# Optimization experiments

Measured on AMD Instinct MI355X. Metric: run time of the kernel, lower is better.

Reference implementation:

```python
import jax, jax.numpy as jnp
import numpy as np

BOS = 1          # BOS_TOK_IDX
PAD = 0          # PAD_TOK_IDX (embedding padding row zeroed)
NL = 2           # n_layers (both decoder and encoder)
H_DEC = 1024     # decoder hidden = enc.emb_size
H_ENC = 512      # encoder hidden per direction (out_size = 1024)


def lstm_cell(x, h, c, Wih, Whh, bih, bhh):
    # PyTorch gate order: i, f, g, o
    gates = x @ Wih.T + h @ Whh.T + bih + bhh
    i, f, g, o = jnp.split(gates, 4, axis=-1)
    c = jax.nn.sigmoid(f) * c + jax.nn.sigmoid(i) * jnp.tanh(g)
    h = jax.nn.sigmoid(o) * jnp.tanh(c)
    return h, c


def setup_inputs() -> dict:
    key = jax.random.key(0)
    ks = jax.random.split(key, 20)
    B, T_ENC, V, E = 32, 128, 32000, 512
    sd = 1.0 / np.sqrt(H_DEC)
    se = 1.0 / np.sqrt(H_ENC)
    u = lambda k, shape, s: jax.random.uniform(k, shape, jnp.float32, -s, s)
    emb_W = jax.random.normal(ks[0], (V, E), jnp.float32)
    emb_W = emb_W.at[PAD].set(0.0)  # padding_idx
    return {
        "enc_outs": jax.random.normal(ks[1], (B, T_ENC, 2 * H_ENC), jnp.float32),
        "enc_h": 0.1 * jax.random.normal(ks[2], (NL, B, H_DEC), jnp.float32),
        "enc_c": 0.1 * jax.random.normal(ks[3], (NL, B, H_DEC), jnp.float32),
        "max_len": 256,
        "emb_W": emb_W,
        # decoder LSTM (unidirectional, 2 layers; layer0 in=E, layer1 in=H_DEC)
        "dec_Wih0": u(ks[4], (4 * H_DEC, E), sd),
        "dec_Whh0": u(ks[5], (4 * H_DEC, H_DEC), sd),
        "dec_bih0": u(ks[6], (4 * H_DEC,), sd),
        "dec_bhh0": u(ks[7], (4 * H_DEC,), sd),
        "dec_Wih1": u(ks[8], (4 * H_DEC, H_DEC), sd),
        "dec_Whh1": u(ks[9], (4 * H_DEC, H_DEC), sd),
        "dec_bih1": u(ks[10], (4 * H_DEC,), sd),
        "dec_bhh1": u(ks[11], (4 * H_DEC,), sd),
        # encoder biLSTM, stacked [layer, dir]; input dim 1024 for both layers
        "enc_Wih": u(ks[12], (NL, 2, 4 * H_ENC, 2 * H_ENC), se),
        "enc_Whh": u(ks[13], (NL, 2, 4 * H_ENC, H_ENC), se),
        "enc_bih": u(ks[14], (NL, 2, 4 * H_ENC), se),
        "enc_bhh": u(ks[15], (NL, 2, 4 * H_ENC), se),
    }


def _run_dir(x, Wih, Whh, bih, bhh, reverse):
    # x: [B, T, D] -> ys: [B, T, H], final (h, c)
    B = x.shape[0]
    H = Whh.shape[-1]
    z = jnp.zeros((B, H), dtype=x.dtype)

    def step(carry, xt):
        h, c = lstm_cell(xt, carry[0], carry[1], Wih, Whh, bih, bhh)
        return (h, c), h

    (hT, cT), ys = jax.lax.scan(step, (z, z), jnp.swapaxes(x, 0, 1), reverse=reverse)
    return jnp.swapaxes(ys, 0, 1), hT, cT


def reference(enc_outs, enc_h, enc_c, max_len, emb_W,
              dec_Wih0, dec_Whh0, dec_bih0, dec_bhh0,
              dec_Wih1, dec_Whh1, dec_bih1, dec_bhh1,
              enc_Wih, enc_Whh, enc_bih, enc_bhh):
    B = enc_outs.shape[0]
    # dec_inps is never updated in the loop: always the BOS embedding (eval dropout = id)
    x0 = jnp.broadcast_to(emb_W[BOS], (B, emb_W.shape[1]))

    def dec_step(carry, _):
        h0, c0, h1, c1 = carry
        h0, c0 = lstm_cell(x0, h0, c0, dec_Wih0, dec_Whh0, dec_bih0, dec_bhh0)
        h1, c1 = lstm_cell(h0, h1, c1, dec_Wih1, dec_Whh1, dec_bih1, dec_bhh1)
        return (h0, c0, h1, c1), h1

    init = (enc_h[0], enc_c[0], enc_h[1], enc_c[1])
    _, result = jax.lax.scan(dec_step, init, None, length=max_len)  # [T, B, H_DEC]
    out = jnp.swapaxes(result, 0, 1)  # [B, T, H_DEC]

    # bidirectional encoder over the decoded sequence (pre_embedded, full lengths)
    for l in range(NL):
        yf, hf, cf = _run_dir(out, enc_Wih[l, 0], enc_Whh[l, 0], enc_bih[l, 0], enc_bhh[l, 0], False)
        yb, hb, cb = _run_dir(out, enc_Wih[l, 1], enc_Whh[l, 1], enc_bih[l, 1], enc_bhh[l, 1], True)
        out = jnp.concatenate([yf, yb], axis=-1)

    # to_dec_state: concat last-layer fwd/bwd states, expand over n_layers
    lnhn = jnp.concatenate([hf, hb], axis=1)  # [B, out_size]
    lncn = jnp.concatenate([cf, cb], axis=1)
    dec_h = jnp.broadcast_to(lnhn, (NL,) + lnhn.shape)
    dec_c = jnp.broadcast_to(lncn, (NL,) + lncn.shape)
    return out, dec_h, dec_c
```

## Files before the change

kernel.cpp:

```cpp
#include <hip/hip_runtime.h>


typedef _Float16 f16;
typedef _Float16 hvec8 __attribute__((ext_vector_type(8)));
typedef float fvec4 __attribute__((ext_vector_type(4)));

#define WS_H0   4096
#define WS_H1   135168
#define WS_HE   266240
#define WS_DEC  397312
#define WS_Y0   17174528

__device__ __forceinline__ fvec4 mf(hvec8 a, hvec8 b, fvec4 c) {
    return __builtin_amdgcn_mfma_f32_16x16x32_f16(a, b, c, 0, 0, 0);
}

__device__ __forceinline__ hvec8 ldb8(const float* p) {
    hvec8 h;
#pragma unroll
    for (int j = 0; j < 8; ++j) h[j] = (f16)p[j];
    return h;
}

__device__ __forceinline__ hvec8 lda8(const f16* p) {
    hvec8 v;
    asm volatile("global_load_dwordx4 %0, %1, off sc1" : "=v"(v) : "v"(p));
    return v;
}
__device__ __forceinline__ void vm_wait() {
    asm volatile("s_waitcnt vmcnt(0)" ::: "memory");
    __builtin_amdgcn_sched_barrier(0);
}

__device__ __forceinline__ void st2(f16* p, float a, float b) {
    union { f16 h[2]; unsigned u; } x;
    x.h[0] = (f16)a; x.h[1] = (f16)b;
    __hip_atomic_store((unsigned*)p, x.u, __ATOMIC_RELAXED, __HIP_MEMORY_SCOPE_AGENT);
}

__device__ __forceinline__ float sigf(float x) { return 1.f / (1.f + __expf(-x)); }
__device__ __forceinline__ float thf(float x) {
    x = fminf(15.f, fmaxf(-15.f, x));
    float e = __expf(2.f * x);
    return (e - 1.f) / (e + 1.f);
}

#define RED(t, m, w, n)  red[(((t)*16 + (m))*132) + ((w)*16) + (n)]
#define RED2(t, m, n)    red2[(((t)*16 + (m))*20) + (n)]

__global__ void __launch_bounds__(512, 1)
seq2seq_kernel(const float* __restrict__ enc_h, const float* __restrict__ enc_c,
               const float* __restrict__ emb_W,
               const float* __restrict__ dWih0, const float* __restrict__ dWhh0,
               const float* __restrict__ dbih0, const float* __restrict__ dbhh0,
               const float* __restrict__ dWih1, const float* __restrict__ dWhh1,
               const float* __restrict__ dbih1, const float* __restrict__ dbhh1,
               const float* __restrict__ eWih, const float* __restrict__ eWhh,
               const float* __restrict__ ebih, const float* __restrict__ ebhh,
               float* __restrict__ out, char* __restrict__ ws)
{
    const int tid  = threadIdx.x;
    const int wave = tid >> 6, lane = tid & 63;
    const int wg   = blockIdx.x;
    const int bg   = wg >> 7;
    const int g    = wg & 127;
    const int n16  = lane & 15;
    const int kq   = (lane >> 4) * 8;

    unsigned* flags  = (unsigned*)ws;
    unsigned* myflag = flags + (size_t)wg * 4;

    f16* H0  = (f16*)(ws + WS_H0);
    f16* H1  = (f16*)(ws + WS_H1);
    f16* HE  = (f16*)(ws + WS_HE);
    f16* DEC = (f16*)(ws + WS_DEC);
    f16* Y0  = (f16*)(ws + WS_Y0);

    __shared__ float red[64 * 132];
    __shared__ float red2[64 * 20];
    __shared__ float cdec[2][8][16];
    __shared__ float cenc[8][16];
    __shared__ float pre0_l[32];
    __shared__ float bias1_l[32];
    __shared__ float biasE_l[32];

    unsigned cnt = 0;
    auto bar = [&](int base, int two) {
        const unsigned tgt = ++cnt;
        __syncthreads();
        if (wave == 0) {
            if (lane == 0)
                __hip_atomic_store(myflag, tgt, __ATOMIC_RELAXED, __HIP_MEMORY_SCOPE_AGENT);
            const unsigned* p0 = flags + (size_t)(base + lane) * 4;
            const unsigned* p1 = p0 + 64 * 4;
            for (;;) {
                unsigned a = __hip_atomic_load(p0, __ATOMIC_RELAXED, __HIP_MEMORY_SCOPE_AGENT);
                if (two) {
                    unsigned b = __hip_atomic_load(p1, __ATOMIC_RELAXED, __HIP_MEMORY_SCOPE_AGENT);
                    a = (a < b) ? a : b;
                }
                if (__all((int)(a >= tgt))) break;
                __builtin_amdgcn_s_sleep(2);
            }
        }
        __syncthreads();
    };

    const int u0 = g * 8;
    hvec8 bL0[2][4], bL1[2][8];
    {
        const int gate = n16 >> 2, uu = n16 & 3;
#pragma unroll
        for (int t = 0; t < 2; ++t) {
            const int r = gate * 1024 + u0 + t * 4 + uu;
#pragma unroll
            for (int s = 0; s < 4; ++s)
                bL0[t][s] = ldb8(dWhh0 + (size_t)r * 1024 + wave * 128 + s * 32 + kq);
#pragma unroll
            for (int s = 0; s < 8; ++s) {
                const int k1 = wave * 256 + s * 32;
                bL1[t][s] = (k1 < 1024)
                    ? ldb8(dWih1 + (size_t)r * 1024 + k1 + kq)
                    : ldb8(dWhh1 + (size_t)r * 1024 + (k1 - 1024) + kq);
            }
        }
    }
    if (tid < 128) {
        const int which = tid >> 6, q = tid & 63, j = q >> 4, m = q & 15;
        const int b = bg * 16 + m, u = u0 + 2 * j;
        const float* src_c = enc_c + (size_t)(which * 32 + b) * 1024 + u;
        const float* src_h = enc_h + (size_t)(which * 32 + b) * 1024 + u;
        cdec[which][2 * j][m]     = src_c[0];
        cdec[which][2 * j + 1][m] = src_c[1];
        f16* dst = which ? H1 : H0;
        st2(dst + (size_t)(32 + b) * 1024 + u, src_h[0], src_h[1]);
    }
    if (tid < 32) {
        const int t = tid >> 4, nn = tid & 15;
        const int r = (nn >> 2) * 1024 + u0 + t * 4 + (nn & 3);
        const float* x0 = emb_W + 512;
        float s = dbih0[r] + dbhh0[r];
        const float* wr = dWih0 + (size_t)r * 512;
        for (int k = 0; k < 512; ++k) s += wr[k] * x0[k];
        pre0_l[tid]  = s;
        bias1_l[tid] = dbih1[r] + dbhh1[r];
    }
    bar(bg * 128, 1);

    for (int tau = 0; tau <= 256; ++tau) {
        const int prd = (tau + 1) & 1;
        const int pwr = tau & 1;
        fvec4 acc[4];
#pragma unroll
        for (int i = 0; i < 4; ++i) acc[i] = 0;
        const int m = n16;
        hvec8 a0f[4], a1f[8];
        if (tau < 256) {
            const f16* a0 = H0 + (size_t)(prd * 32 + bg * 16 + m) * 1024 + wave * 128 + kq;
#pragma unroll
            for (int s = 0; s < 4; ++s) a0f[s] = lda8(a0 + s * 32);
        }
        if (tau >= 1) {
            const f16* a1 = (wave < 4)
                ? H0 + (size_t)(prd * 32 + bg * 16 + m) * 1024 + wave * 256 + kq
                : H1 + (size_t)(pwr * 32 + bg * 16 + m) * 1024 + (wave - 4) * 256 + kq;
#pragma unroll
            for (int s = 0; s < 8; ++s) a1f[s] = lda8(a1 + s * 32);
        }
        vm_wait();
        if (tau < 256) {
#pragma unroll
            for (int s = 0; s < 4; ++s) {
                acc[0] = mf(a0f[s], bL0[0][s], acc[0]);
                acc[1] = mf(a0f[s], bL0[1][s], acc[1]);
            }
        }
        if (tau >= 1) {
#pragma unroll
            for (int s = 0; s < 8; ++s) {
                acc[2] = mf(a1f[s], bL1[0][s], acc[2]);
                acc[3] = mf(a1f[s], bL1[1][s], acc[3]);
            }
        }
        {
            const int mg = lane >> 4;
#pragma unroll
            for (int t = 0; t < 4; ++t)
#pragma unroll
                for (int r = 0; r < 4; ++r)
                    RED(t, mg * 4 + r, wave, n16) = acc[t][r];
        }
        __syncthreads();
        for (int it = tid; it < 1024; it += 512) {
            const int t = it >> 8, mm = it & 15, nn = (it >> 4) & 15;
            const float* p = &RED(t, mm, 0, nn);
            RED2(t, mm, nn) = ((p[0] + p[16]) + (p[32] + p[48]))
                            + ((p[64] + p[80]) + (p[96] + p[112]));
        }
        __syncthreads();
        if (tid < 64 && tau < 256) {
            const int j = tid >> 4, m2 = tid & 15, t = j >> 1;
            float hh[2];
#pragma unroll
            for (int e = 0; e < 2; ++e) {
                const int uu = 2 * j + e, ul = uu & 3;
                const float gi = RED2(t, m2, ul)      + pre0_l[t * 16 + ul];
                const float gf = RED2(t, m2, 4 + ul)  + pre0_l[t * 16 + 4 + ul];
                const float gg = RED2(t, m2, 8 + ul)  + pre0_l[t * 16 + 8 + ul];
                const float go = RED2(t, m2, 12 + ul) + pre0_l[t * 16 + 12 + ul];
                float c = cdec[0][uu][m2];
                c = sigf(gf) * c + sigf(gi) * thf(gg);
                hh[e] = sigf(go) * thf(c);
                cdec[0][uu][m2] = c;
            }
            st2(H0 + (size_t)(pwr * 32 + bg * 16 + m2) * 1024 + u0 + 2 * j, hh[0], hh[1]);
        }
        if (tid >= 64 && tid < 128 && tau >= 1) {
            const int q = tid - 64;
            const int j = q >> 4, m2 = q & 15, t = j >> 1;
            float hh[2];
#pragma unroll
            for (int e = 0; e < 2; ++e) {
                const int uu = 2 * j + e, ul = uu & 3;
                const float gi = RED2(2 + t, m2, ul)      + bias1_l[t * 16 + ul];
                const float gf = RED2(2 + t, m2, 4 + ul)  + bias1_l[t * 16 + 4 + ul];
                const float gg = RED2(2 + t, m2, 8 + ul)  + bias1_l[t * 16 + 8 + ul];
                const float go = RED2(2 + t, m2, 12 + ul) + bias1_l[t * 16 + 12 + ul];
                float c = cdec[1][uu][m2];
                c = sigf(gf) * c + sigf(gi) * thf(gg);
                hh[e] = sigf(go) * thf(c);
                cdec[1][uu][m2] = c;
            }
            const int b = bg * 16 + m2, u = u0 + 2 * j;
            st2(H1 + (size_t)(prd * 32 + b) * 1024 + u, hh[0], hh[1]);
            st2(DEC + ((size_t)(tau - 1) * 32 + b) * 1024 + u, hh[0], hh[1]);
        }
        bar(bg * 128, 1);
    }

    const int dir = g >> 6;
    const int ge  = g & 63;
    const int ue0 = ge * 8;
    const int dbase = bg * 128 + dir * 64;
    for (int l = 0; l < 2; ++l) {
        hvec8 bE[2][6];
        {
            const int gate = n16 >> 2, uu = n16 & 3;
            const float* Wih = eWih + (size_t)(l * 2 + dir) * 2048 * 1024;
            const float* Whh = eWhh + (size_t)(l * 2 + dir) * 2048 * 512;
#pragma unroll
            for (int t = 0; t < 2; ++t) {
                const int r = gate * 512 + ue0 + t * 4 + uu;
#pragma unroll
                for (int s = 0; s < 6; ++s) {
                    const int kb = wave * 192 + s * 32;
                    bE[t][s] = (kb < 1024)
                        ? ldb8(Wih + (size_t)r * 1024 + kb + kq)
                        : ldb8(Whh + (size_t)r * 512 + (kb - 1024) + kq);
                }
            }
        }
        if (tid < 32) {
            const int t = tid >> 4, nn = tid & 15;
            const int r = (nn >> 2) * 512 + ue0 + t * 4 + (nn & 3);
            biasE_l[tid] = ebih[(size_t)(l * 2 + dir) * 2048 + r]
                         + ebhh[(size_t)(l * 2 + dir) * 2048 + r];
        }
        if (tid < 64) {
            const int j = tid >> 4, m = tid & 15;
            cenc[2 * j][m] = 0.f;
            cenc[2 * j + 1][m] = 0.f;
            st2(HE + (size_t)((dir * 2 + 1) * 32 + bg * 16 + m) * 512 + ue0 + 2 * j, 0.f, 0.f);
        }
        bar(dbase, 0);
        const f16* yprev = (l == 0) ? DEC : Y0;
        for (int tau = 0; tau < 256; ++tau) {
            const int t = dir ? (255 - tau) : tau;
            const int prd = (tau + 1) & 1, pwr = tau & 1;
            fvec4 acc2[2];
            acc2[0] = 0; acc2[1] = 0;
            const int m = n16, b = bg * 16 + m;
            hvec8 aef[6];
#pragma unroll
            for (int s = 0; s < 6; ++s) {
                const int kb = wave * 192 + s * 32;
                const f16* p = (kb < 1024)
                    ? yprev + ((size_t)t * 32 + b) * 1024 + kb + kq
                    : HE + (size_t)((dir * 2 + prd) * 32 + b) * 512 + (kb - 1024) + kq;
                aef[s] = lda8(p);
            }
            vm_wait();
#pragma unroll
            for (int s = 0; s < 6; ++s) {
                acc2[0] = mf(aef[s], bE[0][s], acc2[0]);
                acc2[1] = mf(aef[s], bE[1][s], acc2[1]);
            }
            const int mg = lane >> 4;
#pragma unroll
            for (int tt = 0; tt < 2; ++tt)
#pragma unroll
                for (int r = 0; r < 4; ++r)
                    RED(tt, mg * 4 + r, wave, n16) = acc2[tt][r];
            __syncthreads();
            {
                const int t2 = tid >> 8, mm = tid & 15, nn = (tid >> 4) & 15;
                const float* p = &RED(t2, mm, 0, nn);
                RED2(t2, mm, nn) = ((p[0] + p[16]) + (p[32] + p[48]))
                                 + ((p[64] + p[80]) + (p[96] + p[112]));
            }
            __syncthreads();
            if (tid < 64) {
                const int j = tid >> 4, m2 = tid & 15, tt = j >> 1;
                float hh[2], cc[2];
#pragma unroll
                for (int e = 0; e < 2; ++e) {
                    const int uu = 2 * j + e, ul = uu & 3;
                    const float gi = RED2(tt, m2, ul)      + biasE_l[tt * 16 + ul];
                    const float gf = RED2(tt, m2, 4 + ul)  + biasE_l[tt * 16 + 4 + ul];
                    const float gg = RED2(tt, m2, 8 + ul)  + biasE_l[tt * 16 + 8 + ul];
                    const float go = RED2(tt, m2, 12 + ul) + biasE_l[tt * 16 + 12 + ul];
                    float c = cenc[uu][m2];
                    c = sigf(gf) * c + sigf(gi) * thf(gg);
                    hh[e] = sigf(go) * thf(c);
                    cc[e] = c;
                    cenc[uu][m2] = c;
                }
                const int b2 = bg * 16 + m2, u = ue0 + 2 * j;
                st2(HE + (size_t)((dir * 2 + pwr) * 32 + b2) * 512 + u, hh[0], hh[1]);
                if (l == 0) {
                    st2(Y0 + ((size_t)t * 32 + b2) * 1024 + dir * 512 + u, hh[0], hh[1]);
                } else {
                    float* o = out + ((size_t)b2 * 256 + t) * 1024 + dir * 512 + u;
                    o[0] = hh[0]; o[1] = hh[1];
                    if (tau == 255) {
                        const int col = dir * 512 + u;
                        float* oh = out + 8388608 + (size_t)b2 * 1024 + col;
                        float* oc = out + 8454144 + (size_t)b2 * 1024 + col;
                        oh[0] = hh[0]; oh[1] = hh[1];
                        oh[32768] = hh[0]; oh[32769] = hh[1];
                        oc[0] = cc[0]; oc[1] = cc[1];
                        oc[32768] = cc[0]; oc[32769] = cc[1];
                    }
                }
            }
            bar(dbase, 0);
        }
        if (l == 0) bar(bg * 128, 1);
    }
}

extern "C" void kernel_launch(void* const* d_in, const int* in_sizes, int n_in,
                              void* d_out, int out_size, void* d_ws, size_t ws_size,
                              hipStream_t stream) {
    (void)in_sizes; (void)n_in; (void)out_size; (void)ws_size;
    const float* enc_h = (const float*)d_in[1];
    const float* enc_c = (const float*)d_in[2];
    const float* emb_W = (const float*)d_in[4];
    const float* dWih0 = (const float*)d_in[5];
    const float* dWhh0 = (const float*)d_in[6];
    const float* dbih0 = (const float*)d_in[7];
    const float* dbhh0 = (const float*)d_in[8];
    const float* dWih1 = (const float*)d_in[9];
    const float* dWhh1 = (const float*)d_in[10];
    const float* dbih1 = (const float*)d_in[11];
    const float* dbhh1 = (const float*)d_in[12];
    const float* eWih  = (const float*)d_in[13];
    const float* eWhh  = (const float*)d_in[14];
    const float* ebih  = (const float*)d_in[15];
    const float* ebhh  = (const float*)d_in[16];
    float* outp = (float*)d_out;
    char* ws = (char*)d_ws;

    hipMemsetAsync(d_ws, 0, 4096, stream);

    void* args[] = {&enc_h, &enc_c, &emb_W, &dWih0, &dWhh0, &dbih0, &dbhh0,
                    &dWih1, &dWhh1, &dbih1, &dbhh1, &eWih, &eWhh, &ebih, &ebhh,
                    &outp, &ws};
    hipLaunchCooperativeKernel((const void*)seq2seq_kernel, dim3(256), dim3(512),
                               args, 0, stream);
}
```

Baseline: 3.795 ms.

## Halve encoder workgroups, fuse cross-wave reduction into gate math, prefetch encoder inputs

The encoder phase now runs on 128 workgroups instead of 256, each owning 16 hidden units (four MFMA column tiles) so per-step grid barriers span 32 groups rather than 64. The separate RED2 reduction pass and its extra __syncthreads are removed; the threads doing the gate math sum the eight wave partials directly from shared memory. Next-timestep encoder inputs are prefetched into registers during the current step's MFMAs, and the barrier spin-loop no longer sleeps. The trade-offs are more register pressure, more work per group on the serial recurrence, and half the groups idling through the encoder.

```diff
diff --git a/kernel.cpp b/kernel.cpp
--- a/kernel.cpp
+++ b/kernel.cpp
@@ -46,7 +46,10 @@
 }
 
 #define RED(t, m, w, n)  red[(((t)*16 + (m))*132) + ((w)*16) + (n)]
-#define RED2(t, m, n)    red2[(((t)*16 + (m))*20) + (n)]
+
+__device__ __forceinline__ float sum8(const float* p) {
+    return ((p[0] + p[16]) + (p[32] + p[48])) + ((p[64] + p[80]) + (p[96] + p[112]));
+}
 
 __global__ void __launch_bounds__(512, 1)
 seq2seq_kernel(const float* __restrict__ enc_h, const float* __restrict__ enc_c,
@@ -77,30 +80,33 @@
     f16* Y0  = (f16*)(ws + WS_Y0);
 
     __shared__ float red[64 * 132];
-    __shared__ float red2[64 * 20];
     __shared__ float cdec[2][8][16];
-    __shared__ float cenc[8][16];
+    __shared__ float cenc[16][16];
     __shared__ float pre0_l[32];
     __shared__ float bias1_l[32];
-    __shared__ float biasE_l[32];
+    __shared__ float biasE_l[64];
 
     unsigned cnt = 0;
-    auto bar = [&](int base, int two) {
+    auto bar = [&](int base, int width) {
         const unsigned tgt = ++cnt;
         __syncthreads();
         if (wave == 0) {
             if (lane == 0)
                 __hip_atomic_store(myflag, tgt, __ATOMIC_RELAXED, __HIP_MEMORY_SCOPE_AGENT);
-            const unsigned* p0 = flags + (size_t)(base + lane) * 4;
-            const unsigned* p1 = p0 + 64 * 4;
+            const unsigned* p0 = flags + (size_t)(base + (lane & (width - 1))) * 4;
             for (;;) {
                 unsigned a = __hip_atomic_load(p0, __ATOMIC_RELAXED, __HIP_MEMORY_SCOPE_AGENT);
-                if (two) {
-                    unsigned b = __hip_atomic_load(p1, __ATOMIC_RELAXED, __HIP_MEMORY_SCOPE_AGENT);
-                    a = (a < b) ? a : b;
+                if (width > 64) {
+                    unsigned b = __hip_atomic_load(p0 + 64 * 4, __ATOMIC_RELAXED, __HIP_MEMORY_SCOPE_AGENT);
+                    a = a < b ? a : b;
+                    if (width > 128) {
+                        unsigned c2 = __hip_atomic_load(p0 + 128 * 4, __ATOMIC_RELAXED, __HIP_MEMORY_SCOPE_AGENT);
+                        unsigned d2 = __hip_atomic_load(p0 + 192 * 4, __ATOMIC_RELAXED, __HIP_MEMORY_SCOPE_AGENT);
+                        a = a < c2 ? a : c2;
+                        a = a < d2 ? a : d2;
+                    }
                 }
                 if (__all((int)(a >= tgt))) break;
-                __builtin_amdgcn_s_sleep(2);
             }
         }
         __syncthreads();
@@ -145,7 +151,7 @@
         pre0_l[tid]  = s;
         bias1_l[tid] = dbih1[r] + dbhh1[r];
     }
-    bar(bg * 128, 1);
+    bar(bg * 128, 128);
 
     for (int tau = 0; tau <= 256; ++tau) {
         const int prd = (tau + 1) & 1;
@@ -191,23 +197,17 @@
                     RED(t, mg * 4 + r, wave, n16) = acc[t][r];
         }
         __syncthreads();
-        for (int it = tid; it < 1024; it += 512) {
-            const int t = it >> 8, mm = it & 15, nn = (it >> 4) & 15;
-            const float* p = &RED(t, mm, 0, nn);
-            RED2(t, mm, nn) = ((p[0] + p[16]) + (p[32] + p[48]))
-                            + ((p[64] + p[80]) + (p[96] + p[112]));
-        }
-        __syncthreads();
         if (tid < 64 && tau < 256) {
             const int j = tid >> 4, m2 = tid & 15, t = j >> 1;
             float hh[2];
 #pragma unroll
             for (int e = 0; e < 2; ++e) {
                 const int uu = 2 * j + e, ul = uu & 3;
-                const float gi = RED2(t, m2, ul)      + pre0_l[t * 16 + ul];
-                const float gf = RED2(t, m2, 4 + ul)  + pre0_l[t * 16 + 4 + ul];
-                const float gg = RED2(t, m2, 8 + ul)  + pre0_l[t * 16 + 8 + ul];
-                const float go = RED2(t, m2, 12 + ul) + pre0_l[t * 16 + 12 + ul];
+                const float* p = &RED(t, m2, 0, ul);
+                const float gi = sum8(p)      + pre0_l[t * 16 + ul];
+                const float gf = sum8(p + 4)  + pre0_l[t * 16 + 4 + ul];
+                const float gg = sum8(p + 8)  + pre0_l[t * 16 + 8 + ul];
+                const float go = sum8(p + 12) + pre0_l[t * 16 + 12 + ul];
                 float c = cdec[0][uu][m2];
                 c = sigf(gf) * c + sigf(gi) * thf(gg);
                 hh[e] = sigf(go) * thf(c);
@@ -222,10 +222,11 @@
 #pragma unroll
             for (int e = 0; e < 2; ++e) {
                 const int uu = 2 * j + e, ul = uu & 3;
-                const float gi = RED2(2 + t, m2, ul)      + bias1_l[t * 16 + ul];
-                const float gf = RED2(2 + t, m2, 4 + ul)  + bias1_l[t * 16 + 4 + ul];
-                const float gg = RED2(2 + t, m2, 8 + ul)  + bias1_l[t * 16 + 8 + ul];
-                const float go = RED2(2 + t, m2, 12 + ul) + bias1_l[t * 16 + 12 + ul];
+                const float* p = &RED(2 + t, m2, 0, ul);
+                const float gi = sum8(p)      + bias1_l[t * 16 + ul];
+                const float gf = sum8(p + 4)  + bias1_l[t * 16 + 4 + ul];
+                const float gg = sum8(p + 8)  + bias1_l[t * 16 + 8 + ul];
+                const float go = sum8(p + 12) + bias1_l[t * 16 + 12 + ul];
                 float c = cdec[1][uu][m2];
                 c = sigf(gf) * c + sigf(gi) * thf(gg);
                 hh[e] = sigf(go) * thf(c);
@@ -235,21 +236,25 @@
             st2(H1 + (size_t)(prd * 32 + b) * 1024 + u, hh[0], hh[1]);
             st2(DEC + ((size_t)(tau - 1) * 32 + b) * 1024 + u, hh[0], hh[1]);
         }
-        bar(bg * 128, 1);
+        bar(bg * 128, 128);
     }
 
-    const int dir = g >> 6;
-    const int ge  = g & 63;
-    const int ue0 = ge * 8;
-    const int dbase = bg * 128 + dir * 64;
+    bar(0, 256);
+    if (wg >= 128) return;
+
+    const int bg2 = wg >> 6;
+    const int dir = (wg >> 5) & 1;
+    const int ge  = wg & 31;
+    const int ue0 = ge * 16;
+    const int dbase = bg2 * 64 + dir * 32;
     for (int l = 0; l < 2; ++l) {
-        hvec8 bE[2][6];
+        hvec8 bE[4][6];
         {
             const int gate = n16 >> 2, uu = n16 & 3;
             const float* Wih = eWih + (size_t)(l * 2 + dir) * 2048 * 1024;
             const float* Whh = eWhh + (size_t)(l * 2 + dir) * 2048 * 512;
 #pragma unroll
-            for (int t = 0; t < 2; ++t) {
+            for (int t = 0; t < 4; ++t) {
                 const int r = gate * 512 + ue0 + t * 4 + uu;
 #pragma unroll
                 for (int s = 0; s < 6; ++s) {
@@ -260,72 +265,89 @@
                 }
             }
         }
-        if (tid < 32) {
+        if (tid < 64) {
             const int t = tid >> 4, nn = tid & 15;
             const int r = (nn >> 2) * 512 + ue0 + t * 4 + (nn & 3);
             biasE_l[tid] = ebih[(size_t)(l * 2 + dir) * 2048 + r]
                          + ebhh[(size_t)(l * 2 + dir) * 2048 + r];
         }
-        if (tid < 64) {
+        if (tid < 128) {
             const int j = tid >> 4, m = tid & 15;
             cenc[2 * j][m] = 0.f;
             cenc[2 * j + 1][m] = 0.f;
-            st2(HE + (size_t)((dir * 2 + 1) * 32 + bg * 16 + m) * 512 + ue0 + 2 * j, 0.f, 0.f);
-        }
-        bar(dbase, 0);
+            st2(HE + (size_t)((dir * 2 + 1) * 32 + bg2 * 16 + m) * 512 + ue0 + 2 * j, 0.f, 0.f);
+        }
+        bar(dbase, 32);
         const f16* yprev = (l == 0) ? DEC : Y0;
+        hvec8 ypf[6];
+        {
+            const int t0 = dir ? 255 : 0;
+            const int b = bg2 * 16 + n16;
+#pragma unroll
+            for (int s = 0; s < 6; ++s) {
+                const int kb = wave * 192 + s * 32;
+                if (kb < 1024)
+                    ypf[s] = lda8(yprev + ((size_t)t0 * 32 + b) * 1024 + kb + kq);
+            }
+        }
         for (int tau = 0; tau < 256; ++tau) {
             const int t = dir ? (255 - tau) : tau;
             const int prd = (tau + 1) & 1, pwr = tau & 1;
-            fvec4 acc2[2];
-            acc2[0] = 0; acc2[1] = 0;
-            const int m = n16, b = bg * 16 + m;
-            hvec8 aef[6];
+            const int b = bg2 * 16 + n16;
+            hvec8 hef[6];
 #pragma unroll
             for (int s = 0; s < 6; ++s) {
                 const int kb = wave * 192 + s * 32;
-                const f16* p = (kb < 1024)
-                    ? yprev + ((size_t)t * 32 + b) * 1024 + kb + kq
-                    : HE + (size_t)((dir * 2 + prd) * 32 + b) * 512 + (kb - 1024) + kq;
-                aef[s] = lda8(p);
+                if (kb >= 1024)
+                    hef[s] = lda8(HE + (size_t)((dir * 2 + prd) * 32 + b) * 512 + (kb - 1024) + kq);
             }
             vm_wait();
+            fvec4 acc2[4];
+#pragma unroll
+            for (int i = 0; i < 4; ++i) acc2[i] = 0;
 #pragma unroll
             for (int s = 0; s < 6; ++s) {
-                acc2[0] = mf(aef[s], bE[0][s], acc2[0]);
-                acc2[1] = mf(aef[s], bE[1][s], acc2[1]);
+                const int kb = wave * 192 + s * 32;
+                const hvec8 a = (kb < 1024) ? ypf[s] : hef[s];
+                acc2[0] = mf(a, bE[0][s], acc2[0]);
+                acc2[1] = mf(a, bE[1][s], acc2[1]);
+                acc2[2] = mf(a, bE[2][s], acc2[2]);
+                acc2[3] = mf(a, bE[3][s], acc2[3]);
+            }
+            if (tau < 255) {
+                const int tn = dir ? (t - 1) : (t + 1);
+#pragma unroll
+                for (int s = 0; s < 6; ++s) {
+                    const int kb = wave * 192 + s * 32;
+                    if (kb < 1024)
+                        ypf[s] = lda8(yprev + ((size_t)tn * 32 + b) * 1024 + kb + kq);
+                }
             }
             const int mg = lane >> 4;
 #pragma unroll
-            for (int tt = 0; tt < 2; ++tt)
+            for (int tt = 0; tt < 4; ++tt)
 #pragma unroll
                 for (int r = 0; r < 4; ++r)
                     RED(tt, mg * 4 + r, wave, n16) = acc2[tt][r];
             __syncthreads();
-            {
-                const int t2 = tid >> 8, mm = tid & 15, nn = (tid >> 4) & 15;
-                const float* p = &RED(t2, mm, 0, nn);
-                RED2(t2, mm, nn) = ((p[0] + p[16]) + (p[32] + p[48]))
-                                 + ((p[64] + p[80]) + (p[96] + p[112]));
-            }
-            __syncthreads();
-            if (tid < 64) {
-                const int j = tid >> 4, m2 = tid & 15, tt = j >> 1;
+            if (tid < 128) {
+                const int j = tid >> 4, m2 = tid & 15;
                 float hh[2], cc[2];
 #pragma unroll
                 for (int e = 0; e < 2; ++e) {
-                    const int uu = 2 * j + e, ul = uu & 3;
-                    const float gi = RED2(tt, m2, ul)      + biasE_l[tt * 16 + ul];
-                    const float gf = RED2(tt, m2, 4 + ul)  + biasE_l[tt * 16 + 4 + ul];
-                    const float gg = RED2(tt, m2, 8 + ul)  + biasE_l[tt * 16 + 8 + ul];
-                    const float go = RED2(tt, m2, 12 + ul) + biasE_l[tt * 16 + 12 + ul];
+                    const int uu = 2 * j + e, tt = uu >> 2, ul = uu & 3;
+                    const float* p = &RED(tt, m2, 0, ul);
+                    const float gi = sum8(p)      + biasE_l[tt * 16 + ul];
+                    const float gf = sum8(p + 4)  + biasE_l[tt * 16 + 4 + ul];
+                    const float gg = sum8(p + 8)  + biasE_l[tt * 16 + 8 + ul];
+                    const float go = sum8(p + 12) + biasE_l[tt * 16 + 12 + ul];
                     float c = cenc[uu][m2];
                     c = sigf(gf) * c + sigf(gi) * thf(gg);
                     hh[e] = sigf(go) * thf(c);
                     cc[e] = c;
                     cenc[uu][m2] = c;
                 }
-                const int b2 = bg * 16 + m2, u = ue0 + 2 * j;
+                const int b2 = bg2 * 16 + m2, u = ue0 + 2 * j;
                 st2(HE + (size_t)((dir * 2 + pwr) * 32 + b2) * 512 + u, hh[0], hh[1]);
                 if (l == 0) {
                     st2(Y0 + ((size_t)t * 32 + b2) * 1024 + dir * 512 + u, hh[0], hh[1]);
@@ -343,9 +365,9 @@
                     }
                 }
             }
-            bar(dbase, 0);
-        }
-        if (l == 0) bar(bg * 128, 1);
+            bar(dbase, 32);
+        }
+        if (l == 0) bar(bg2 * 64, 64);
     }
 }
 
```

Result: no change. 3.791 ms (-0.1%).
